# Kernel optimization log

Measured on AMD Instinct MI355X. Metric: run time of the kernel, lower is better.

The kernel has to match this reference:

```python
import jax, jax.numpy as jnp
import numpy as np

SINKHORN_ITERS = 20
EPS = 1e-8


def sinkhorn(M):
    # Normalize |M| to doubly-stochastic via alternating row/col normalization.
    A = jnp.abs(M) + EPS
    def body(i, A):
        A = A / jnp.sum(A, axis=1, keepdims=True)
        A = A / jnp.sum(A, axis=0, keepdims=True)
        return A
    return jax.lax.fori_loop(0, SINKHORN_ITERS, body, A)


def setup_inputs() -> dict:
    key = jax.random.key(0)
    k1, k2 = jax.random.split(key)
    n_streams = 4
    B, T, D = 4, 4096, 1024
    x = jax.random.normal(k1, (B, T, n_streams, D), dtype=jnp.float32)
    # init_identity=True: eye + 0.01 * noise
    H_raw = jnp.eye(n_streams, dtype=jnp.float32) + 0.01 * jax.random.normal(k2, (n_streams, n_streams), dtype=jnp.float32)
    return {"x": x, "H_raw": H_raw}


def reference(x, H_raw):
    H = sinkhorn(H_raw)  # [n, m] doubly stochastic
    # mix residual streams: [n,m] x [b,t,m,d] -> [b,t,n,d]
    return jnp.einsum('nm,btmd->btnd', H, x)
```

## Files before the change

### kernel.cpp

```cpp
#include <hip/hip_runtime.h>

#define SINKHORN_ITERS 20
#define N_STREAMS 4
#define DDIM 1024

__global__ void sinkhorn_k(const float* __restrict__ H_raw, float* __restrict__ H) {
    if (blockIdx.x == 0 && threadIdx.x == 0) {
        float A[4][4];
#pragma unroll
        for (int i = 0; i < 4; ++i)
#pragma unroll
            for (int j = 0; j < 4; ++j)
                A[i][j] = fabsf(H_raw[i * 4 + j]) + 1e-8f;

        for (int it = 0; it < SINKHORN_ITERS; ++it) {
#pragma unroll
            for (int i = 0; i < 4; ++i) {
                float r = A[i][0] + A[i][1] + A[i][2] + A[i][3];
                float rinv = 1.0f / r;
#pragma unroll
                for (int j = 0; j < 4; ++j) A[i][j] *= rinv;
            }
#pragma unroll
            for (int j = 0; j < 4; ++j) {
                float c = A[0][j] + A[1][j] + A[2][j] + A[3][j];
                float cinv = 1.0f / c;
#pragma unroll
                for (int i = 0; i < 4; ++i) A[i][j] *= cinv;
            }
        }
#pragma unroll
        for (int i = 0; i < 4; ++i)
#pragma unroll
            for (int j = 0; j < 4; ++j)
                H[i * 4 + j] = A[i][j];
    }
}

__global__ __launch_bounds__(256) void mix_k(const float* __restrict__ x,
                                             const float* __restrict__ H,
                                             float* __restrict__ out,
                                             int n_items ) {
    int idx = blockIdx.x * 256 + threadIdx.x;
    if (idx >= n_items) return;
    int bt = idx >> 8;
    int dv = idx & 255;

    const float4* xp = (const float4*)(x) + (size_t)bt * (N_STREAMS * DDIM / 4) + dv;
    float4* op = (float4*)(out) + (size_t)bt * (N_STREAMS * DDIM / 4) + dv;

    float h[16];
#pragma unroll
    for (int i = 0; i < 16; ++i) h[i] = H[i];

    const int C = DDIM / 4;
    float4 x0 = xp[0 * C];
    float4 x1 = xp[1 * C];
    float4 x2 = xp[2 * C];
    float4 x3 = xp[3 * C];

#pragma unroll
    for (int n = 0; n < 4; ++n) {
        float4 o;
        o.x = h[n * 4 + 0] * x0.x + h[n * 4 + 1] * x1.x + h[n * 4 + 2] * x2.x + h[n * 4 + 3] * x3.x;
        o.y = h[n * 4 + 0] * x0.y + h[n * 4 + 1] * x1.y + h[n * 4 + 2] * x2.y + h[n * 4 + 3] * x3.y;
        o.z = h[n * 4 + 0] * x0.z + h[n * 4 + 1] * x1.z + h[n * 4 + 2] * x2.z + h[n * 4 + 3] * x3.z;
        o.w = h[n * 4 + 0] * x0.w + h[n * 4 + 1] * x1.w + h[n * 4 + 2] * x2.w + h[n * 4 + 3] * x3.w;
        op[n * C] = o;
    }
}

extern "C" void kernel_launch(void* const* d_in, const int* in_sizes, int n_in,
                              void* d_out, int out_size, void* d_ws, size_t ws_size,
                              hipStream_t stream) {
    const float* x = (const float*)d_in[0];
    const float* H_raw = (const float*)d_in[1];
    float* out = (float*)d_out;
    float* H = (float*)d_ws;

    sinkhorn_k<<<1, 64, 0, stream>>>(H_raw, H);

    int n_items = in_sizes[0] / (N_STREAMS * 4);
    int blocks = (n_items + 255) / 256;
    mix_k<<<blocks, 256, 0, stream>>>(x, H, out, n_items);
}
```

Before: 437.2 us.

## Fuse Sinkhorn into mix kernel with wave-shuffle normalization and multi-row blocks

Drops the separate single-thread Sinkhorn launch. Each wavefront now recomputes the 4x4 doubly-stochastic matrix in registers, using lane shuffles for the row and column sums, then broadcasts it to all lanes. Each block also processes 8 (b,t) rows in a loop, which spreads the redundant Sinkhorn work over more data and cuts the block count. The cost is roughly 20 serial shuffle and divide iterations at the start of every block, plus less memory-level parallelism per thread because the row loop is not unrolled.

```diff
diff --git a/kernel.cpp b/kernel.cpp
--- a/kernel.cpp
+++ b/kernel.cpp
@@ -3,70 +3,54 @@
 #define SINKHORN_ITERS 20
 #define N_STREAMS 4
 #define DDIM 1024
+#define BT_PER_BLOCK 8
 
-__global__ void sinkhorn_k(const float* __restrict__ H_raw, float* __restrict__ H) {
-    if (blockIdx.x == 0 && threadIdx.x == 0) {
-        float A[4][4];
-#pragma unroll
-        for (int i = 0; i < 4; ++i)
-#pragma unroll
-            for (int j = 0; j < 4; ++j)
-                A[i][j] = fabsf(H_raw[i * 4 + j]) + 1e-8f;
+__global__ __launch_bounds__(256) void fused_mix_k(const float* __restrict__ x,
+                                                   const float* __restrict__ H_raw,
+                                                   float* __restrict__ out,
+                                                   int n_bt) {
+    const int tid = threadIdx.x;
+    const int lane = tid & 63;
 
-        for (int it = 0; it < SINKHORN_ITERS; ++it) {
-#pragma unroll
-            for (int i = 0; i < 4; ++i) {
-                float r = A[i][0] + A[i][1] + A[i][2] + A[i][3];
-                float rinv = 1.0f / r;
-#pragma unroll
-                for (int j = 0; j < 4; ++j) A[i][j] *= rinv;
-            }
-#pragma unroll
-            for (int j = 0; j < 4; ++j) {
-                float c = A[0][j] + A[1][j] + A[2][j] + A[3][j];
-                float cinv = 1.0f / c;
-#pragma unroll
-                for (int i = 0; i < 4; ++i) A[i][j] *= cinv;
-            }
-        }
-#pragma unroll
-        for (int i = 0; i < 4; ++i)
-#pragma unroll
-            for (int j = 0; j < 4; ++j)
-                H[i * 4 + j] = A[i][j];
+    float A = fabsf(H_raw[lane & 15]) + 1e-8f;
+#pragma unroll 1
+    for (int it = 0; it < SINKHORN_ITERS; ++it) {
+        float r1 = A + __shfl_xor(A, 1);
+        float rs = r1 + __shfl_xor(r1, 2);
+        A = A / rs;
+        float c1 = A + __shfl_xor(A, 4);
+        float cs = c1 + __shfl_xor(c1, 8);
+        A = A / cs;
     }
-}
-
-__global__ __launch_bounds__(256) void mix_k(const float* __restrict__ x,
-                                             const float* __restrict__ H,
-                                             float* __restrict__ out,
-                                             int n_items ) {
-    int idx = blockIdx.x * 256 + threadIdx.x;
-    if (idx >= n_items) return;
-    int bt = idx >> 8;
-    int dv = idx & 255;
-
-    const float4* xp = (const float4*)(x) + (size_t)bt * (N_STREAMS * DDIM / 4) + dv;
-    float4* op = (float4*)(out) + (size_t)bt * (N_STREAMS * DDIM / 4) + dv;
-
     float h[16];
 #pragma unroll
-    for (int i = 0; i < 16; ++i) h[i] = H[i];
+    for (int k = 0; k < 16; ++k) h[k] = __shfl(A, k);
 
     const int C = DDIM / 4;
-    float4 x0 = xp[0 * C];
-    float4 x1 = xp[1 * C];
-    float4 x2 = xp[2 * C];
-    float4 x3 = xp[3 * C];
+    const int dv = tid;
+    int bt0 = blockIdx.x * BT_PER_BLOCK;
+
+#pragma unroll 1
+    for (int g = 0; g < BT_PER_BLOCK; ++g) {
+        int bt = bt0 + g;
+        if (bt >= n_bt) break;
+        const float4* xp = (const float4*)x + (size_t)bt * (N_STREAMS * C) + dv;
+        float4* op = (float4*)out + (size_t)bt * (N_STREAMS * C) + dv;
+
+        float4 x0 = xp[0 * C];
+        float4 x1 = xp[1 * C];
+        float4 x2 = xp[2 * C];
+        float4 x3 = xp[3 * C];
 
 #pragma unroll
-    for (int n = 0; n < 4; ++n) {
-        float4 o;
-        o.x = h[n * 4 + 0] * x0.x + h[n * 4 + 1] * x1.x + h[n * 4 + 2] * x2.x + h[n * 4 + 3] * x3.x;
-        o.y = h[n * 4 + 0] * x0.y + h[n * 4 + 1] * x1.y + h[n * 4 + 2] * x2.y + h[n * 4 + 3] * x3.y;
-        o.z = h[n * 4 + 0] * x0.z + h[n * 4 + 1] * x1.z + h[n * 4 + 2] * x2.z + h[n * 4 + 3] * x3.z;
-        o.w = h[n * 4 + 0] * x0.w + h[n * 4 + 1] * x1.w + h[n * 4 + 2] * x2.w + h[n * 4 + 3] * x3.w;
-        op[n * C] = o;
+        for (int n = 0; n < 4; ++n) {
+            float4 o;
+            o.x = h[n*4+0]*x0.x + h[n*4+1]*x1.x + h[n*4+2]*x2.x + h[n*4+3]*x3.x;
+            o.y = h[n*4+0]*x0.y + h[n*4+1]*x1.y + h[n*4+2]*x2.y + h[n*4+3]*x3.y;
+            o.z = h[n*4+0]*x0.z + h[n*4+1]*x1.z + h[n*4+2]*x2.z + h[n*4+3]*x3.z;
+            o.w = h[n*4+0]*x0.w + h[n*4+1]*x1.w + h[n*4+2]*x2.w + h[n*4+3]*x3.w;
+            op[n * C] = o;
+        }
     }
 }
 
@@ -76,11 +60,8 @@
     const float* x = (const float*)d_in[0];
     const float* H_raw = (const float*)d_in[1];
     float* out = (float*)d_out;
-    float* H = (float*)d_ws;
 
-    sinkhorn_k<<<1, 64, 0, stream>>>(H_raw, H);
-
-    int n_items = in_sizes[0] / (N_STREAMS * 4);
-    int blocks = (n_items + 255) / 256;
-    mix_k<<<blocks, 256, 0, stream>>>(x, H, out, n_items);
+    int n_bt = in_sizes[0] / (N_STREAMS * DDIM);
+    int blocks = (n_bt + BT_PER_BLOCK - 1) / BT_PER_BLOCK;
+    fused_mix_k<<<blocks, 256, 0, stream>>>(x, H_raw, out, n_bt);
 }
```

Measured after the change: 443.9 us. About the same (+1.5%).
